# Kernel tuning notes

Measured on AMD Instinct MI355X. Metric: run time of the kernel, lower is better.

## Reference

```python
import jax, jax.numpy as jnp
import numpy as np

NUM_QUBITS = 12
DIM = 2 ** NUM_QUBITS  # 4096
BATCH = 2048
TWO_PI = 2.0 * np.pi


def _diag_phases(p0, p1):
    """Kronecker product of per-qubit diag(exp(i*p0[k]), exp(i*p1[k])) matrices,
    represented as the length-2^n diagonal vector. Phases add under kron of
    diagonal exponentials, so accumulate phases and exponentiate once."""
    ph = jnp.zeros((1,), jnp.float32)
    n = p0.shape[0]
    for k in range(n):  # loop over qubits (small, structural)
        ph = (ph[:, None] + jnp.stack([p0[k], p1[k]])[None, :]).reshape(-1)
    return jnp.exp(1j * ph)  # complex64 diagonal of the 2^n x 2^n operator


def _bs_matrix(n):
    """n-fold Kronecker product of the 50/50 beamsplitter matrix."""
    inv_sqrt2 = np.float32(1.0 / np.sqrt(2.0))
    bs = jnp.array([[1.0, 1j], [1j, 1.0]], dtype=jnp.complex64) * inv_sqrt2
    M = jnp.ones((1, 1), dtype=jnp.complex64)
    for _ in range(n):
        M = jnp.kron(M, bs)
    return M  # [2^n, 2^n]


def setup_inputs() -> dict:
    key = jax.random.key(0)
    k1, k2, k3, k4, k5, k6 = jax.random.split(key, 6)
    return {
        "x_real": jax.random.normal(k1, (BATCH, DIM), dtype=jnp.float32),
        "x_imag": jax.random.normal(k2, (BATCH, DIM), dtype=jnp.float32),
        "alphas": jax.random.uniform(k3, (NUM_QUBITS,), dtype=jnp.float32, maxval=TWO_PI),
        "betas": jax.random.uniform(k4, (NUM_QUBITS,), dtype=jnp.float32, maxval=TWO_PI),
        "thetas": jax.random.uniform(k5, (NUM_QUBITS,), dtype=jnp.float32, maxval=TWO_PI),
        "phis": jax.random.uniform(k6, (NUM_QUBITS,), dtype=jnp.float32, maxval=TWO_PI),
    }


def reference(x_real, x_imag, alphas, betas, thetas, phis):
    x = x_real + 1j * x_imag  # [B, 2^n] complex64
    zeros = jnp.zeros_like(thetas)
    d_in = _diag_phases(alphas, betas)   # input_shifts diagonal
    d_th = _diag_phases(thetas, zeros)   # theta_shifts diagonal
    d_ph = _diag_phases(phis, zeros)     # phi_shifts diagonal
    bs = _bs_matrix(NUM_QUBITS)          # dense tensor-product matrix
    # K.dot(x, M) == x @ M; diagonal matmuls become row-wise elementwise scales.
    out = (x * d_in) @ bs
    out = (out * d_th) @ bs
    out = out * d_ph
    return out
```

## Files before the change

### kernel.cpp

```cpp
#include <hip/hip_runtime.h>
#include <math.h>

#define NQ 12
#define DIM 4096
#define BATCH 2048

typedef float fv4 __attribute__((ext_vector_type(4)));

#if defined(__has_builtin)
#if __has_builtin(__builtin_nontemporal_load) && __has_builtin(__builtin_nontemporal_store)
#define NT_LOAD(p)     __builtin_nontemporal_load(p)
#define NT_STORE(p, v) __builtin_nontemporal_store((v), (p))
#endif
#endif
#ifndef NT_LOAD
#define NT_LOAD(p)     (*(p))
#define NT_STORE(p, v) (*(p) = (v))
#endif

__device__ __forceinline__ int swz(int e) { return e ^ ((e >> 4) & 15); }

__device__ __forceinline__ float2 cmul(float2 a, float2 b) {
    return make_float2(a.x * b.x - a.y * b.y, a.x * b.y + a.y * b.x);
}

__device__ __forceinline__ void bf4(float (&vr)[16], float (&vi)[16]) {
#pragma unroll
    for (int m = 1; m < 16; m <<= 1) {
#pragma unroll
        for (int r = 0; r < 16; ++r) {
            if (r & m) continue;
            const int p = r | m;
            float ur = vr[r], ui = vi[r], wr = vr[p], wi = vi[p];
            vr[r] = ur - wi;  vi[r] = ui + wr;
            vr[p] = wr - ui;  vi[p] = wi + ur;
        }
    }
}

template <bool INTERLEAVED>
__global__ __launch_bounds__(256, 4) void qlayer(
        const float* __restrict__ xr, const float* __restrict__ xi,
        const float* __restrict__ alphas, const float* __restrict__ betas,
        const float* __restrict__ thetas, const float* __restrict__ phis,
        float* __restrict__ out) {
    __shared__ float2 lds[DIM];
    __shared__ float2 hi_in[64], lo_in[64];
    __shared__ float2 hi_th[64], lo_th[64];
    __shared__ float2 hi_ph[64], lo_ph[64];

    const int row = blockIdx.x;
    const int t = threadIdx.x;

    const float* xrp = xr + (size_t)row * DIM;
    const float* xip = xi + (size_t)row * DIM;

    fv4 re[4], im[4];
#pragma unroll
    for (int c = 0; c < 4; ++c) {
        const int e0 = (c << 10) + (t << 2);
        re[c] = NT_LOAD(reinterpret_cast<const fv4*>(xrp + e0));
        im[c] = NT_LOAD(reinterpret_cast<const fv4*>(xip + e0));
    }

    if (t < 64) {
        float p_in = 0.f, p_th = 0.f, p_ph = 0.f;
#pragma unroll
        for (int k = 0; k < 6; ++k) {
            if ((t >> (5 - k)) & 1) {
                p_in += betas[k];
            } else {
                p_in += alphas[k]; p_th += thetas[k]; p_ph += phis[k];
            }
        }
        const float g = 1.0f / 64.0f;
        float s, c;
        sincosf(p_in, &s, &c); hi_in[t] = make_float2(c, s);
        sincosf(p_th, &s, &c); hi_th[t] = make_float2(c * g, s * g);
        sincosf(p_ph, &s, &c); hi_ph[t] = make_float2(c * g, s * g);
    } else if (t < 128) {
        const int l = t - 64;
        float p_in = 0.f, p_th = 0.f, p_ph = 0.f;
#pragma unroll
        for (int k = 6; k < 12; ++k) {
            if ((l >> (11 - k)) & 1) {
                p_in += betas[k];
            } else {
                p_in += alphas[k]; p_th += thetas[k]; p_ph += phis[k];
            }
        }
        float s, c;
        sincosf(p_in, &s, &c); lo_in[l] = make_float2(c, s);
        sincosf(p_th, &s, &c); lo_th[l] = make_float2(c, s);
        sincosf(p_ph, &s, &c); lo_ph[l] = make_float2(c, s);
    }
    __syncthreads();

    float vr[16], vi[16];

    float2 fin[4];
#pragma unroll
    for (int j = 0; j < 4; ++j) fin[j] = lo_in[((t & 15) << 2) | j];
#pragma unroll
    for (int c = 0; c < 4; ++c) {
        const float2 fhi = hi_in[(c << 4) | (t >> 4)];
#pragma unroll
        for (int j = 0; j < 4; ++j) {
            const float2 d = cmul(fhi, fin[j]);
            const float rr = re[c][j], ii = im[c][j];
            vr[c * 4 + j] = rr * d.x - ii * d.y;
            vi[c * 4 + j] = rr * d.y + ii * d.x;
        }
    }

    bf4(vr, vi);

#pragma unroll
    for (int r = 0; r < 16; ++r) {
        const int e = ((r >> 2) << 10) | (t << 2) | (r & 3);
        lds[swz(e)] = make_float2(vr[r], vi[r]);
    }
    __syncthreads();
#pragma unroll
    for (int r = 0; r < 16; ++r) {
        const int e = ((t >> 2) << 6) | (r << 2) | (t & 3);
        float2 v = lds[swz(e)];
        vr[r] = v.x; vi[r] = v.y;
    }
    __syncthreads();

    bf4(vr, vi);

#pragma unroll
    for (int r = 0; r < 16; ++r) {
        const int e = ((t >> 2) << 6) | (r << 2) | (t & 3);
        lds[swz(e)] = make_float2(vr[r], vi[r]);
    }
    __syncthreads();
#pragma unroll
    for (int r = 0; r < 16; ++r) {
        const int e = ((t >> 6) << 10) | (r << 6) | (t & 63);
        float2 v = lds[swz(e)];
        vr[r] = v.x; vi[r] = v.y;
    }
    __syncthreads();

    bf4(vr, vi);

    {
        const float2 flo = lo_th[t & 63];
#pragma unroll
        for (int r = 0; r < 16; ++r) {
            const float2 d = cmul(hi_th[((t >> 6) << 4) | r], flo);
            const float a = vr[r], b = vi[r];
            vr[r] = a * d.x - b * d.y;
            vi[r] = a * d.y + b * d.x;
        }
    }

    bf4(vr, vi);

#pragma unroll
    for (int r = 0; r < 16; ++r) {
        const int e = ((t >> 6) << 10) | (r << 6) | (t & 63);
        lds[swz(e)] = make_float2(vr[r], vi[r]);
    }
    __syncthreads();
#pragma unroll
    for (int r = 0; r < 16; ++r) {
        const int e = ((t >> 2) << 6) | (r << 2) | (t & 3);
        float2 v = lds[swz(e)];
        vr[r] = v.x; vi[r] = v.y;
    }
    __syncthreads();

    bf4(vr, vi);

#pragma unroll
    for (int r = 0; r < 16; ++r) {
        const int e = ((t >> 2) << 6) | (r << 2) | (t & 3);
        lds[swz(e)] = make_float2(vr[r], vi[r]);
    }
    __syncthreads();
#pragma unroll
    for (int r = 0; r < 16; ++r) {
        const int e = ((r >> 2) << 10) | (t << 2) | (r & 3);
        float2 v = lds[swz(e)];
        vr[r] = v.x; vi[r] = v.y;
    }

    bf4(vr, vi);

    float2 fph[4];
#pragma unroll
    for (int j = 0; j < 4; ++j) fph[j] = lo_ph[((t & 15) << 2) | j];

    if (INTERLEAVED) {
        float* outp = out + (size_t)row * DIM * 2;
#pragma unroll
        for (int c = 0; c < 4; ++c) {
            const int e0 = (c << 10) + (t << 2);
            const float2 fhi = hi_ph[(c << 4) | (t >> 4)];
            fv4 o0, o1;
#pragma unroll
            for (int j = 0; j < 4; ++j) {
                const float2 d = cmul(fhi, fph[j]);
                const float a = vr[c * 4 + j], b = vi[c * 4 + j];
                const float orr = a * d.x - b * d.y;
                const float oii = a * d.y + b * d.x;
                if (j < 2) { o0[2 * j] = orr; o0[2 * j + 1] = oii; }
                else       { o1[2 * (j - 2)] = orr; o1[2 * (j - 2) + 1] = oii; }
            }
            NT_STORE(reinterpret_cast<fv4*>(outp + 2 * e0), o0);
            NT_STORE(reinterpret_cast<fv4*>(outp + 2 * e0 + 4), o1);
        }
    } else {
        float* outp = out + (size_t)row * DIM;
#pragma unroll
        for (int c = 0; c < 4; ++c) {
            const int e0 = (c << 10) + (t << 2);
            const float2 fhi = hi_ph[(c << 4) | (t >> 4)];
            fv4 o;
#pragma unroll
            for (int j = 0; j < 4; ++j) {
                const float2 d = cmul(fhi, fph[j]);
                o[j] = vr[c * 4 + j] * d.x - vi[c * 4 + j] * d.y;
            }
            NT_STORE(reinterpret_cast<fv4*>(outp + e0), o);
        }
    }
}

extern "C" void kernel_launch(void* const* d_in, const int* in_sizes, int n_in,
                              void* d_out, int out_size, void* d_ws, size_t ws_size,
                              hipStream_t stream) {
    const float* xr     = (const float*)d_in[0];
    const float* xi     = (const float*)d_in[1];
    const float* alphas = (const float*)d_in[2];
    const float* betas  = (const float*)d_in[3];
    const float* thetas = (const float*)d_in[4];
    const float* phis   = (const float*)d_in[5];

    if (out_size >= 2 * BATCH * DIM) {
        qlayer<true><<<BATCH, 256, 0, stream>>>(xr, xi, alphas, betas, thetas,
                                                phis, (float*)d_out);
    } else {
        qlayer<false><<<BATCH, 256, 0, stream>>>(xr, xi, alphas, betas, thetas,
                                                 phis, (float*)d_out);
    }
}
```

Before: 121.5 us.

## Process two rows per block and prefetch next row during transform

Each block now handles two batch rows (grid halved). Phase tables are computed once per block and reused across both rows. The next row's input is loaded mid-transform so global loads overlap with compute. The cost is extra registers from holding the prefetched data alongside the working state, which may lower occupancy, and fewer blocks to spread across the GPU.

After: 134.2 us. +10.5%, slower.

```diff
diff --git a/kernel.cpp b/kernel.cpp
--- a/kernel.cpp
+++ b/kernel.cpp
@@ -4,6 +4,8 @@
 #define NQ 12
 #define DIM 4096
 #define BATCH 2048
+#define RPB 2
+#define GRID (BATCH / RPB)
 
 typedef float fv4 __attribute__((ext_vector_type(4)));
 
@@ -49,18 +51,19 @@
     __shared__ float2 hi_th[64], lo_th[64];
     __shared__ float2 hi_ph[64], lo_ph[64];
 
-    const int row = blockIdx.x;
     const int t = threadIdx.x;
-
-    const float* xrp = xr + (size_t)row * DIM;
-    const float* xip = xi + (size_t)row * DIM;
+    const int row0 = blockIdx.x;
 
     fv4 re[4], im[4];
-#pragma unroll
-    for (int c = 0; c < 4; ++c) {
-        const int e0 = (c << 10) + (t << 2);
-        re[c] = NT_LOAD(reinterpret_cast<const fv4*>(xrp + e0));
-        im[c] = NT_LOAD(reinterpret_cast<const fv4*>(xip + e0));
+    {
+        const float* xrp = xr + (size_t)row0 * DIM;
+        const float* xip = xi + (size_t)row0 * DIM;
+#pragma unroll
+        for (int c = 0; c < 4; ++c) {
+            const int e0 = (c << 10) + (t << 2);
+            re[c] = NT_LOAD(reinterpret_cast<const fv4*>(xrp + e0));
+            im[c] = NT_LOAD(reinterpret_cast<const fv4*>(xip + e0));
+        }
     }
 
     if (t < 64) {
@@ -98,135 +101,145 @@
 
     float vr[16], vi[16];
 
-    float2 fin[4];
-#pragma unroll
-    for (int j = 0; j < 4; ++j) fin[j] = lo_in[((t & 15) << 2) | j];
-#pragma unroll
-    for (int c = 0; c < 4; ++c) {
-        const float2 fhi = hi_in[(c << 4) | (t >> 4)];
-#pragma unroll
-        for (int j = 0; j < 4; ++j) {
-            const float2 d = cmul(fhi, fin[j]);
-            const float rr = re[c][j], ii = im[c][j];
-            vr[c * 4 + j] = rr * d.x - ii * d.y;
-            vi[c * 4 + j] = rr * d.y + ii * d.x;
-        }
-    }
-
-    bf4(vr, vi);
-
-#pragma unroll
-    for (int r = 0; r < 16; ++r) {
-        const int e = ((r >> 2) << 10) | (t << 2) | (r & 3);
-        lds[swz(e)] = make_float2(vr[r], vi[r]);
-    }
-    __syncthreads();
-#pragma unroll
-    for (int r = 0; r < 16; ++r) {
-        const int e = ((t >> 2) << 6) | (r << 2) | (t & 3);
-        float2 v = lds[swz(e)];
-        vr[r] = v.x; vi[r] = v.y;
-    }
-    __syncthreads();
-
-    bf4(vr, vi);
-
-#pragma unroll
-    for (int r = 0; r < 16; ++r) {
-        const int e = ((t >> 2) << 6) | (r << 2) | (t & 3);
-        lds[swz(e)] = make_float2(vr[r], vi[r]);
-    }
-    __syncthreads();
-#pragma unroll
-    for (int r = 0; r < 16; ++r) {
-        const int e = ((t >> 6) << 10) | (r << 6) | (t & 63);
-        float2 v = lds[swz(e)];
-        vr[r] = v.x; vi[r] = v.y;
-    }
-    __syncthreads();
-
-    bf4(vr, vi);
-
-    {
-        const float2 flo = lo_th[t & 63];
-#pragma unroll
-        for (int r = 0; r < 16; ++r) {
-            const float2 d = cmul(hi_th[((t >> 6) << 4) | r], flo);
-            const float a = vr[r], b = vi[r];
-            vr[r] = a * d.x - b * d.y;
-            vi[r] = a * d.y + b * d.x;
-        }
-    }
-
-    bf4(vr, vi);
-
-#pragma unroll
-    for (int r = 0; r < 16; ++r) {
-        const int e = ((t >> 6) << 10) | (r << 6) | (t & 63);
-        lds[swz(e)] = make_float2(vr[r], vi[r]);
-    }
-    __syncthreads();
-#pragma unroll
-    for (int r = 0; r < 16; ++r) {
-        const int e = ((t >> 2) << 6) | (r << 2) | (t & 3);
-        float2 v = lds[swz(e)];
-        vr[r] = v.x; vi[r] = v.y;
-    }
-    __syncthreads();
-
-    bf4(vr, vi);
-
-#pragma unroll
-    for (int r = 0; r < 16; ++r) {
-        const int e = ((t >> 2) << 6) | (r << 2) | (t & 3);
-        lds[swz(e)] = make_float2(vr[r], vi[r]);
-    }
-    __syncthreads();
-#pragma unroll
-    for (int r = 0; r < 16; ++r) {
-        const int e = ((r >> 2) << 10) | (t << 2) | (r & 3);
-        float2 v = lds[swz(e)];
-        vr[r] = v.x; vi[r] = v.y;
-    }
-
-    bf4(vr, vi);
-
-    float2 fph[4];
-#pragma unroll
-    for (int j = 0; j < 4; ++j) fph[j] = lo_ph[((t & 15) << 2) | j];
-
-    if (INTERLEAVED) {
-        float* outp = out + (size_t)row * DIM * 2;
+#pragma unroll
+    for (int it = 0; it < RPB; ++it) {
+        const int row = row0 + it * GRID;
+        if (it) __syncthreads();
+
 #pragma unroll
         for (int c = 0; c < 4; ++c) {
-            const int e0 = (c << 10) + (t << 2);
-            const float2 fhi = hi_ph[(c << 4) | (t >> 4)];
-            fv4 o0, o1;
+            const float2 fhi = hi_in[(c << 4) | (t >> 4)];
 #pragma unroll
             for (int j = 0; j < 4; ++j) {
-                const float2 d = cmul(fhi, fph[j]);
-                const float a = vr[c * 4 + j], b = vi[c * 4 + j];
-                const float orr = a * d.x - b * d.y;
-                const float oii = a * d.y + b * d.x;
-                if (j < 2) { o0[2 * j] = orr; o0[2 * j + 1] = oii; }
-                else       { o1[2 * (j - 2)] = orr; o1[2 * (j - 2) + 1] = oii; }
-            }
-            NT_STORE(reinterpret_cast<fv4*>(outp + 2 * e0), o0);
-            NT_STORE(reinterpret_cast<fv4*>(outp + 2 * e0 + 4), o1);
-        }
-    } else {
-        float* outp = out + (size_t)row * DIM;
-#pragma unroll
-        for (int c = 0; c < 4; ++c) {
-            const int e0 = (c << 10) + (t << 2);
-            const float2 fhi = hi_ph[(c << 4) | (t >> 4)];
-            fv4 o;
-#pragma unroll
-            for (int j = 0; j < 4; ++j) {
-                const float2 d = cmul(fhi, fph[j]);
-                o[j] = vr[c * 4 + j] * d.x - vi[c * 4 + j] * d.y;
-            }
-            NT_STORE(reinterpret_cast<fv4*>(outp + e0), o);
+                const float2 d = cmul(fhi, lo_in[((t & 15) << 2) | j]);
+                const float rr = re[c][j], ii = im[c][j];
+                vr[c * 4 + j] = rr * d.x - ii * d.y;
+                vi[c * 4 + j] = rr * d.y + ii * d.x;
+            }
+        }
+
+        bf4(vr, vi);
+
+#pragma unroll
+        for (int r = 0; r < 16; ++r) {
+            const int e = ((r >> 2) << 10) | (t << 2) | (r & 3);
+            lds[swz(e)] = make_float2(vr[r], vi[r]);
+        }
+        __syncthreads();
+#pragma unroll
+        for (int r = 0; r < 16; ++r) {
+            const int e = ((t >> 2) << 6) | (r << 2) | (t & 3);
+            float2 v = lds[swz(e)];
+            vr[r] = v.x; vi[r] = v.y;
+        }
+        __syncthreads();
+
+        bf4(vr, vi);
+
+#pragma unroll
+        for (int r = 0; r < 16; ++r) {
+            const int e = ((t >> 2) << 6) | (r << 2) | (t & 3);
+            lds[swz(e)] = make_float2(vr[r], vi[r]);
+        }
+        __syncthreads();
+#pragma unroll
+        for (int r = 0; r < 16; ++r) {
+            const int e = ((t >> 6) << 10) | (r << 6) | (t & 63);
+            float2 v = lds[swz(e)];
+            vr[r] = v.x; vi[r] = v.y;
+        }
+        __syncthreads();
+
+        bf4(vr, vi);
+
+        {
+            const float2 flo = lo_th[t & 63];
+#pragma unroll
+            for (int r = 0; r < 16; ++r) {
+                const float2 d = cmul(hi_th[((t >> 6) << 4) | r], flo);
+                const float a = vr[r], b = vi[r];
+                vr[r] = a * d.x - b * d.y;
+                vi[r] = a * d.y + b * d.x;
+            }
+        }
+
+        bf4(vr, vi);
+
+#pragma unroll
+        for (int r = 0; r < 16; ++r) {
+            const int e = ((t >> 6) << 10) | (r << 6) | (t & 63);
+            lds[swz(e)] = make_float2(vr[r], vi[r]);
+        }
+        __syncthreads();
+#pragma unroll
+        for (int r = 0; r < 16; ++r) {
+            const int e = ((t >> 2) << 6) | (r << 2) | (t & 3);
+            float2 v = lds[swz(e)];
+            vr[r] = v.x; vi[r] = v.y;
+        }
+
+        if (it + 1 < RPB) {
+            const float* xrp = xr + (size_t)(row + GRID) * DIM;
+            const float* xip = xi + (size_t)(row + GRID) * DIM;
+#pragma unroll
+            for (int c = 0; c < 4; ++c) {
+                const int e0 = (c << 10) + (t << 2);
+                re[c] = NT_LOAD(reinterpret_cast<const fv4*>(xrp + e0));
+                im[c] = NT_LOAD(reinterpret_cast<const fv4*>(xip + e0));
+            }
+        }
+        __syncthreads();
+
+        bf4(vr, vi);
+
+#pragma unroll
+        for (int r = 0; r < 16; ++r) {
+            const int e = ((t >> 2) << 6) | (r << 2) | (t & 3);
+            lds[swz(e)] = make_float2(vr[r], vi[r]);
+        }
+        __syncthreads();
+#pragma unroll
+        for (int r = 0; r < 16; ++r) {
+            const int e = ((r >> 2) << 10) | (t << 2) | (r & 3);
+            float2 v = lds[swz(e)];
+            vr[r] = v.x; vi[r] = v.y;
+        }
+
+        bf4(vr, vi);
+
+        if (INTERLEAVED) {
+            float* outp = out + (size_t)row * DIM * 2;
+#pragma unroll
+            for (int c = 0; c < 4; ++c) {
+                const int e0 = (c << 10) + (t << 2);
+                const float2 fhi = hi_ph[(c << 4) | (t >> 4)];
+                fv4 o0, o1;
+#pragma unroll
+                for (int j = 0; j < 4; ++j) {
+                    const float2 d = cmul(fhi, lo_ph[((t & 15) << 2) | j]);
+                    const float a = vr[c * 4 + j], b = vi[c * 4 + j];
+                    const float orr = a * d.x - b * d.y;
+                    const float oii = a * d.y + b * d.x;
+                    if (j < 2) { o0[2 * j] = orr; o0[2 * j + 1] = oii; }
+                    else       { o1[2 * (j - 2)] = orr; o1[2 * (j - 2) + 1] = oii; }
+                }
+                NT_STORE(reinterpret_cast<fv4*>(outp + 2 * e0), o0);
+                NT_STORE(reinterpret_cast<fv4*>(outp + 2 * e0 + 4), o1);
+            }
+        } else {
+            float* outp = out + (size_t)row * DIM;
+#pragma unroll
+            for (int c = 0; c < 4; ++c) {
+                const int e0 = (c << 10) + (t << 2);
+                const float2 fhi = hi_ph[(c << 4) | (t >> 4)];
+                fv4 o;
+#pragma unroll
+                for (int j = 0; j < 4; ++j) {
+                    const float2 d = cmul(fhi, lo_ph[((t & 15) << 2) | j]);
+                    o[j] = vr[c * 4 + j] * d.x - vi[c * 4 + j] * d.y;
+                }
+                NT_STORE(reinterpret_cast<fv4*>(outp + e0), o);
+            }
         }
     }
 }
@@ -242,10 +255,10 @@
     const float* phis   = (const float*)d_in[5];
 
     if (out_size >= 2 * BATCH * DIM) {
-        qlayer<true><<<BATCH, 256, 0, stream>>>(xr, xi, alphas, betas, thetas,
+        qlayer<true><<<GRID, 256, 0, stream>>>(xr, xi, alphas, betas, thetas,
+                                               phis, (float*)d_out);
+    } else {
+        qlayer<false><<<GRID, 256, 0, stream>>>(xr, xi, alphas, betas, thetas,
                                                 phis, (float*)d_out);
-    } else {
-        qlayer<false><<<BATCH, 256, 0, stream>>>(xr, xi, alphas, betas, thetas,
-                                                 phis, (float*)d_out);
-    }
-}
+    }
+}
```

## Fuse both beamsplitter passes into one per-qubit 2x2 gate pass

Applied to the files above, without the earlier changes.

The operator is a Kronecker product of per-qubit factors (diag phases, beamsplitter, theta phase, beamsplitter, phi phase), so each qubit's full chain collapses into a single complex 2x2 matrix. The kernel now applies 12 general 2x2 gates in three radix-16 register stages. The second butterfly sweep, two LDS round trips and the diagonal scaling passes are gone. Each butterfly now costs a full complex 2x2 multiply instead of add/sub only, and output stores are 8-byte strided per thread instead of 16-byte vectors.

After: 160.9 us. +32.4%, slower.

```diff
diff --git a/kernel.cpp b/kernel.cpp
--- a/kernel.cpp
+++ b/kernel.cpp
@@ -6,6 +6,7 @@
 #define BATCH 2048
 
 typedef float fv4 __attribute__((ext_vector_type(4)));
+typedef float fv2 __attribute__((ext_vector_type(2)));
 
 #if defined(__has_builtin)
 #if __has_builtin(__builtin_nontemporal_load) && __has_builtin(__builtin_nontemporal_store)
@@ -20,22 +21,32 @@
 
 __device__ __forceinline__ int swz(int e) { return e ^ ((e >> 4) & 15); }
 
-__device__ __forceinline__ float2 cmul(float2 a, float2 b) {
+__device__ __forceinline__ float2 cmulf(float2 a, float2 b) {
     return make_float2(a.x * b.x - a.y * b.y, a.x * b.y + a.y * b.x);
 }
 
-__device__ __forceinline__ void bf4(float (&vr)[16], float (&vi)[16]) {
+__device__ __forceinline__ void gstage(float (&vr)[16], float (&vi)[16],
+                                       float2 m00, float2 m01,
+                                       float2 m10, float2 m11, int m) {
 #pragma unroll
-    for (int m = 1; m < 16; m <<= 1) {
-#pragma unroll
-        for (int r = 0; r < 16; ++r) {
-            if (r & m) continue;
-            const int p = r | m;
-            float ur = vr[r], ui = vi[r], wr = vr[p], wi = vi[p];
-            vr[r] = ur - wi;  vi[r] = ui + wr;
-            vr[p] = wr - ui;  vi[p] = wi + ur;
-        }
+    for (int r = 0; r < 16; ++r) {
+        if (r & m) continue;
+        const int p = r | m;
+        const float ur = vr[r], ui = vi[r], wr = vr[p], wi = vi[p];
+        vr[r] = ur * m00.x - ui * m00.y + wr * m10.x - wi * m10.y;
+        vi[r] = ur * m00.y + ui * m00.x + wr * m10.y + wi * m10.x;
+        vr[p] = ur * m01.x - ui * m01.y + wr * m11.x - wi * m11.y;
+        vi[p] = ur * m01.y + ui * m01.x + wr * m11.y + wi * m11.x;
     }
+}
+
+__device__ __forceinline__ void gbf4(float (&vr)[16], float (&vi)[16],
+                                     const float2 (*mt)[4],
+                                     int q1, int q2, int q4, int q8) {
+    gstage(vr, vi, mt[q1][0], mt[q1][1], mt[q1][2], mt[q1][3], 1);
+    gstage(vr, vi, mt[q2][0], mt[q2][1], mt[q2][2], mt[q2][3], 2);
+    gstage(vr, vi, mt[q4][0], mt[q4][1], mt[q4][2], mt[q4][3], 4);
+    gstage(vr, vi, mt[q8][0], mt[q8][1], mt[q8][2], mt[q8][3], 8);
 }
 
 template <bool INTERLEAVED>
@@ -45,75 +56,48 @@
         const float* __restrict__ thetas, const float* __restrict__ phis,
         float* __restrict__ out) {
     __shared__ float2 lds[DIM];
-    __shared__ float2 hi_in[64], lo_in[64];
-    __shared__ float2 hi_th[64], lo_th[64];
-    __shared__ float2 hi_ph[64], lo_ph[64];
+    __shared__ float2 mt[NQ][4];
 
+    const int t = threadIdx.x;
     const int row = blockIdx.x;
-    const int t = threadIdx.x;
 
-    const float* xrp = xr + (size_t)row * DIM;
-    const float* xip = xi + (size_t)row * DIM;
-
-    fv4 re[4], im[4];
+    fv4 lre[4], lim[4];
+    {
+        const float* xrp = xr + (size_t)row * DIM;
+        const float* xip = xi + (size_t)row * DIM;
 #pragma unroll
-    for (int c = 0; c < 4; ++c) {
-        const int e0 = (c << 10) + (t << 2);
-        re[c] = NT_LOAD(reinterpret_cast<const fv4*>(xrp + e0));
-        im[c] = NT_LOAD(reinterpret_cast<const fv4*>(xip + e0));
+        for (int c = 0; c < 4; ++c) {
+            const int e0 = (c << 10) + (t << 2);
+            lre[c] = NT_LOAD(reinterpret_cast<const fv4*>(xrp + e0));
+            lim[c] = NT_LOAD(reinterpret_cast<const fv4*>(xip + e0));
+        }
     }
 
-    if (t < 64) {
-        float p_in = 0.f, p_th = 0.f, p_ph = 0.f;
-#pragma unroll
-        for (int k = 0; k < 6; ++k) {
-            if ((t >> (5 - k)) & 1) {
-                p_in += betas[k];
-            } else {
-                p_in += alphas[k]; p_th += thetas[k]; p_ph += phis[k];
-            }
-        }
-        const float g = 1.0f / 64.0f;
+    if (t < NQ) {
+        float sa, ca;
+        sincosf(thetas[t], &sa, &ca);
+        const float2 h0 = make_float2((ca - 1.f) * 0.5f, sa * 0.5f);
+        const float2 h1 = make_float2(-sa * 0.5f, (ca + 1.f) * 0.5f);
+        const float al = alphas[t], be = betas[t], ph = phis[t];
         float s, c;
-        sincosf(p_in, &s, &c); hi_in[t] = make_float2(c, s);
-        sincosf(p_th, &s, &c); hi_th[t] = make_float2(c * g, s * g);
-        sincosf(p_ph, &s, &c); hi_ph[t] = make_float2(c * g, s * g);
-    } else if (t < 128) {
-        const int l = t - 64;
-        float p_in = 0.f, p_th = 0.f, p_ph = 0.f;
-#pragma unroll
-        for (int k = 6; k < 12; ++k) {
-            if ((l >> (11 - k)) & 1) {
-                p_in += betas[k];
-            } else {
-                p_in += alphas[k]; p_th += thetas[k]; p_ph += phis[k];
-            }
-        }
-        float s, c;
-        sincosf(p_in, &s, &c); lo_in[l] = make_float2(c, s);
-        sincosf(p_th, &s, &c); lo_th[l] = make_float2(c, s);
-        sincosf(p_ph, &s, &c); lo_ph[l] = make_float2(c, s);
+        sincosf(al + ph, &s, &c); mt[t][0] = cmulf(make_float2(c, s), h0);
+        sincosf(al, &s, &c);      mt[t][1] = cmulf(make_float2(c, s), h1);
+        sincosf(be + ph, &s, &c); mt[t][2] = cmulf(make_float2(c, s), h1);
+        sincosf(be, &s, &c);      mt[t][3] = cmulf(make_float2(c, s),
+                                                   make_float2(-h0.x, -h0.y));
     }
     __syncthreads();
 
     float vr[16], vi[16];
-
-    float2 fin[4];
 #pragma unroll
-    for (int j = 0; j < 4; ++j) fin[j] = lo_in[((t & 15) << 2) | j];
-#pragma unroll
-    for (int c = 0; c < 4; ++c) {
-        const float2 fhi = hi_in[(c << 4) | (t >> 4)];
+    for (int c = 0; c < 4; ++c)
 #pragma unroll
         for (int j = 0; j < 4; ++j) {
-            const float2 d = cmul(fhi, fin[j]);
-            const float rr = re[c][j], ii = im[c][j];
-            vr[c * 4 + j] = rr * d.x - ii * d.y;
-            vi[c * 4 + j] = rr * d.y + ii * d.x;
+            vr[c * 4 + j] = lre[c][j];
+            vi[c * 4 + j] = lim[c][j];
         }
-    }
 
-    bf4(vr, vi);
+    gbf4(vr, vi, mt, 11, 10, 1, 0);
 
 #pragma unroll
     for (int r = 0; r < 16; ++r) {
@@ -129,7 +113,7 @@
     }
     __syncthreads();
 
-    bf4(vr, vi);
+    gbf4(vr, vi, mt, 9, 8, 7, 6);
 
 #pragma unroll
     for (int r = 0; r < 16; ++r) {
@@ -143,90 +127,23 @@
         float2 v = lds[swz(e)];
         vr[r] = v.x; vi[r] = v.y;
     }
-    __syncthreads();
 
-    bf4(vr, vi);
+    gbf4(vr, vi, mt, 5, 4, 3, 2);
 
-    {
-        const float2 flo = lo_th[t & 63];
+    if (INTERLEAVED) {
+        float2* outp = reinterpret_cast<float2*>(out) + (size_t)row * DIM;
 #pragma unroll
         for (int r = 0; r < 16; ++r) {
-            const float2 d = cmul(hi_th[((t >> 6) << 4) | r], flo);
-            const float a = vr[r], b = vi[r];
-            vr[r] = a * d.x - b * d.y;
-            vi[r] = a * d.y + b * d.x;
-        }
-    }
-
-    bf4(vr, vi);
-
-#pragma unroll
-    for (int r = 0; r < 16; ++r) {
-        const int e = ((t >> 6) << 10) | (r << 6) | (t & 63);
-        lds[swz(e)] = make_float2(vr[r], vi[r]);
-    }
-    __syncthreads();
-#pragma unroll
-    for (int r = 0; r < 16; ++r) {
-        const int e = ((t >> 2) << 6) | (r << 2) | (t & 3);
-        float2 v = lds[swz(e)];
-        vr[r] = v.x; vi[r] = v.y;
-    }
-    __syncthreads();
-
-    bf4(vr, vi);
-
-#pragma unroll
-    for (int r = 0; r < 16; ++r) {
-        const int e = ((t >> 2) << 6) | (r << 2) | (t & 3);
-        lds[swz(e)] = make_float2(vr[r], vi[r]);
-    }
-    __syncthreads();
-#pragma unroll
-    for (int r = 0; r < 16; ++r) {
-        const int e = ((r >> 2) << 10) | (t << 2) | (r & 3);
-        float2 v = lds[swz(e)];
-        vr[r] = v.x; vi[r] = v.y;
-    }
-
-    bf4(vr, vi);
-
-    float2 fph[4];
-#pragma unroll
-    for (int j = 0; j < 4; ++j) fph[j] = lo_ph[((t & 15) << 2) | j];
-
-    if (INTERLEAVED) {
-        float* outp = out + (size_t)row * DIM * 2;
-#pragma unroll
-        for (int c = 0; c < 4; ++c) {
-            const int e0 = (c << 10) + (t << 2);
-            const float2 fhi = hi_ph[(c << 4) | (t >> 4)];
-            fv4 o0, o1;
-#pragma unroll
-            for (int j = 0; j < 4; ++j) {
-                const float2 d = cmul(fhi, fph[j]);
-                const float a = vr[c * 4 + j], b = vi[c * 4 + j];
-                const float orr = a * d.x - b * d.y;
-                const float oii = a * d.y + b * d.x;
-                if (j < 2) { o0[2 * j] = orr; o0[2 * j + 1] = oii; }
-                else       { o1[2 * (j - 2)] = orr; o1[2 * (j - 2) + 1] = oii; }
-            }
-            NT_STORE(reinterpret_cast<fv4*>(outp + 2 * e0), o0);
-            NT_STORE(reinterpret_cast<fv4*>(outp + 2 * e0 + 4), o1);
+            const int e = ((t >> 6) << 10) | (r << 6) | (t & 63);
+            fv2 o; o.x = vr[r]; o.y = vi[r];
+            NT_STORE(reinterpret_cast<fv2*>(outp + e), o);
         }
     } else {
         float* outp = out + (size_t)row * DIM;
 #pragma unroll
-        for (int c = 0; c < 4; ++c) {
-            const int e0 = (c << 10) + (t << 2);
-            const float2 fhi = hi_ph[(c << 4) | (t >> 4)];
-            fv4 o;
-#pragma unroll
-            for (int j = 0; j < 4; ++j) {
-                const float2 d = cmul(fhi, fph[j]);
-                o[j] = vr[c * 4 + j] * d.x - vi[c * 4 + j] * d.y;
-            }
-            NT_STORE(reinterpret_cast<fv4*>(outp + e0), o);
+        for (int r = 0; r < 16; ++r) {
+            const int e = ((t >> 6) << 10) | (r << 6) | (t & 63);
+            NT_STORE(outp + e, vr[r]);
         }
     }
 }
```
